# Performance work log

Hardware: AMD Instinct MI355X
Metric: run time of the kernel (lower is better)

Reference implementation:

```python
import jax, jax.numpy as jnp
import numpy as np

H = 8          # n_heads
THRESH = 0.5   # edge pruning threshold
LN_EPS = 1e-5


def setup_inputs() -> dict:
    key = jax.random.key(0)
    ks = jax.random.split(key, 24)
    B, S, D = 8, 128, 256
    N = S + 1
    hd = D // H

    def lin(k, fan_in, fan_out, gain=1.0):
        # xavier_uniform-ish init, stored as [in, out] (y = x @ W + b)
        lim = gain * np.sqrt(6.0 / (fan_in + fan_out))
        return jax.random.uniform(k, (fan_in, fan_out), jnp.float32, -lim, lim)

    g = 1.0 / np.sqrt(2.0)
    return {
        "desc": jax.random.normal(ks[0], (B, S, D), jnp.float32),
        "nv": jax.random.normal(ks[1], (B, N, D), jnp.float32),
        "W_gt": lin(ks[2], D, D), "b_gt": jnp.zeros((D,), jnp.float32),
        "topo_bias": jnp.zeros((1,), jnp.float32),
        "W_q": lin(ks[3], D, D, g), "b_q": jnp.zeros((D,), jnp.float32),
        "W_k": lin(ks[4], D, D, g), "b_k": jnp.zeros((D,), jnp.float32),
        "W_v": lin(ks[5], D, D, g), "b_v": jnp.zeros((D,), jnp.float32),
        "W_e1": lin(ks[6], 2 * D, D), "b_e1": jnp.zeros((D,), jnp.float32),
        "ln_g": jnp.ones((D,), jnp.float32), "ln_b": jnp.zeros((D,), jnp.float32),
        "W_e2": lin(ks[7], D, D), "b_e2": jnp.zeros((D,), jnp.float32),
        "w_attn": lin(ks[8], 3 * hd, 1, g)[:, 0], "b_attn": jnp.zeros((), jnp.float32),
        "W_o": lin(ks[9], D, D, g), "b_o": jnp.zeros((D,), jnp.float32),
    }


def _forward(desc, nv, W_gt, b_gt, topo_bias, W_q, b_q, W_k, b_k, W_v, b_v,
             W_e1, b_e1, ln_g, ln_b, W_e2, b_e2, w_attn, b_attn, W_o, b_o):
    B, N, D = nv.shape
    S = N - 1
    hd = D // H

    # 1. global topology
    d = desc @ W_gt + b_gt                                   # [B,S,D]
    dn = d / jnp.linalg.norm(d, axis=-1, keepdims=True)
    global_top = jax.nn.sigmoid(jnp.einsum('bid,bjd->bij', dn, dn) + topo_bias[0])

    # 2. sample-wise similarity
    var = nv[:, 1:, :]
    vn = var / jnp.linalg.norm(var, axis=-1, keepdims=True)
    sample_sim = jnp.einsum('bid,bjd->bij', vn, vn)
    adj_mat = global_top * sample_sim

    # 3. remove self-connection, squash
    diag_mask = 1.0 - jnp.eye(S, dtype=adj_mat.dtype)
    adj = jax.nn.sigmoid(adj_mat * diag_mask)

    # 4. straight-through edge pruning (frozen=False path)
    hard = (adj > THRESH).astype(adj.dtype)
    adj = hard - jax.lax.stop_gradient(adj) + adj

    # 5. edge attributes: Linear(concat(d_i,d_j)) decomposed into two matmuls
    a = d @ W_e1[:D]                                          # node_i part [B,S,D]
    b_ = d @ W_e1[D:]                                         # node_j part [B,S,D]
    pre = jnp.zeros((B, N, N, D), dtype=d.dtype)
    pre = pre.at[:, 1:, 1:].set(a[:, :, None, :] + b_[:, None, :, :])
    cls = a + b_                                              # concat(d_j,d_j) rows
    pre = pre.at[:, 0, 1:].set(cls).at[:, 1:, 0].set(cls)
    pre = pre + b_e1                                          # (0,0) entry = bias only (zeros input)
    mu = pre.mean(-1, keepdims=True)
    vr = ((pre - mu) ** 2).mean(-1, keepdims=True)
    e = jax.nn.relu((pre - mu) * jax.lax.rsqrt(vr + LN_EPS) * ln_g + ln_b)
    e = e @ W_e2 + b_e2                                       # [B,N,N,D]
    e = e.reshape(B, N, N, H, hd).transpose(0, 3, 1, 2, 4)    # [B,H,N,N,hd]

    # padded adjacency: CLS row attends to all vars, col 0 masked
    na = jnp.zeros((B, N, N), dtype=adj.dtype)
    na = na.at[:, 1:, 1:].set(adj).at[:, 0, 1:].set(1.0)
    e = e * na[:, None, :, :, None]

    # 6. additive attention: attn_proj(concat(q,k,e)) decomposed
    q = (nv @ W_q + b_q).reshape(B, N, H, hd).transpose(0, 2, 1, 3)
    k = (nv @ W_k + b_k).reshape(B, N, H, hd).transpose(0, 2, 1, 3)
    v = (nv @ W_v + b_v).reshape(B, N, H, hd).transpose(0, 2, 1, 3)
    wq, wk, we = w_attn[:hd], w_attn[hd:2 * hd], w_attn[2 * hd:]
    scores = (jnp.einsum('bhid,d->bhi', q, wq)[:, :, :, None]
              + jnp.einsum('bhjd,d->bhj', k, wk)[:, :, None, :]
              + jnp.einsum('bhijd,d->bhij', e, we) + b_attn)
    scores = scores + (na[:, None, :, :] == 0).astype(scores.dtype) * -1e9
    attn = jax.nn.softmax(scores, axis=-1)                    # dropout = identity (eval)

    ctx = jnp.einsum('bhij,bhjd->bhid', attn, v)
    out = ctx.transpose(0, 2, 1, 3).reshape(B, N, D) @ W_o + b_o
    return out, attn


def reference(desc, nv, W_gt, b_gt, topo_bias, W_q, b_q, W_k, b_k, W_v, b_v,
              W_e1, b_e1, ln_g, ln_b, W_e2, b_e2, w_attn, b_attn, W_o, b_o):
    return _forward(desc, nv, W_gt, b_gt, topo_bias, W_q, b_q, W_k, b_k, W_v, b_v,
                    W_e1, b_e1, ln_g, ln_b, W_e2, b_e2, w_attn, b_attn, W_o, b_o)
```

## Files before the change

### kernel.cpp

```cpp
#include <hip/hip_runtime.h>
#include <math.h>

#define BB 8
#define SS 128
#define NN 129
#define DD 256
#define HH 8
#define LN_EPS 1e-5f

#define OFF_A    0
#define OFF_BPT  262144
#define OFF_CPT  524288
#define OFF_VART 786432
#define OFF_V    1048576
#define OFF_SQ   1312768
#define OFF_SK   1321024
#define OFF_MA   1329280
#define OFF_QA   1330304
#define OFF_MB   1331328
#define OFF_QB   1332352
#define OFF_MC   1333376
#define OFF_QC   1334400
#define OFF_U    1335424
#define OFF_UB   1337472
#define OFF_G    1337600
#define OFF_VV   1468672

struct SA {
    float dsc[4][DD];
    float drow[4][DD];
    float4 red[8][4][64];
    float part[24][4];
};
struct SB {
    float rows[2][DD];
    float4 redq[8][2][64];
    float4 redk[8][2][64];
};
union SMA { SA a; SB b; };

__global__ __launch_bounds__(512) void ka_all(
    const float* __restrict__ desc, const float* __restrict__ nv,
    const float* __restrict__ W_gt, const float* __restrict__ b_gt,
    const float* __restrict__ W_e1, const float* __restrict__ b_e1,
    const float* __restrict__ W_q, const float* __restrict__ b_q,
    const float* __restrict__ W_k, const float* __restrict__ b_k,
    const float* __restrict__ W_v, const float* __restrict__ b_v,
    const float* __restrict__ W_e2, const float* __restrict__ b_e2,
    const float* __restrict__ w_attn,
    float* __restrict__ a, float* __restrict__ bp_t, float* __restrict__ cp_t,
    float* __restrict__ var_t, float* __restrict__ v,
    float* __restrict__ sq, float* __restrict__ sk,
    float* __restrict__ ma, float* __restrict__ qa, float* __restrict__ mb,
    float* __restrict__ qb, float* __restrict__ mc, float* __restrict__ qc,
    float* __restrict__ U, float* __restrict__ ubias) {
    __shared__ SMA sm;
    const int bx = blockIdx.x, t = threadIdx.x;

    if (bx < 256) {
        SA& S = sm.a;
        const int b = bx >> 5, s0 = (bx & 31) * 4;
        const int dq = t & 63, kh = t >> 6;
        for (int e = t; e < 4 * DD; e += 512)
            S.dsc[e >> 8][e & 255] = desc[(size_t)(b * SS + s0 + (e >> 8)) * DD + (e & 255)];
        __syncthreads();
        {
            float4 acc[4];
#pragma unroll
            for (int r = 0; r < 4; r++) acc[r] = make_float4(0.f, 0.f, 0.f, 0.f);
            const int kb = kh * 32;
#pragma unroll 4
            for (int k = kb; k < kb + 32; k++) {
                float4 w = *(const float4*)&W_gt[k * DD + 4 * dq];
#pragma unroll
                for (int r = 0; r < 4; r++) {
                    float x = S.dsc[r][k];
                    acc[r].x = fmaf(x, w.x, acc[r].x); acc[r].y = fmaf(x, w.y, acc[r].y);
                    acc[r].z = fmaf(x, w.z, acc[r].z); acc[r].w = fmaf(x, w.w, acc[r].w);
                }
            }
#pragma unroll
            for (int r = 0; r < 4; r++) S.red[kh][r][dq] = acc[r];
        }
        __syncthreads();
        for (int e = t; e < 4 * DD; e += 512) {
            int r = e >> 8, d2 = e & 255;
            float s = b_gt[d2];
#pragma unroll
            for (int kk = 0; kk < 8; kk++) s += ((const float*)S.red[kk][r])[d2];
            S.drow[r][d2] = s;
        }
        __syncthreads();
        {
            float4 acc[4];
#pragma unroll
            for (int r = 0; r < 4; r++) acc[r] = make_float4(0.f, 0.f, 0.f, 0.f);
            const int kb = kh * 32;
#pragma unroll 4
            for (int k = kb; k < kb + 32; k++) {
                float4 w = *(const float4*)&W_e1[k * DD + 4 * dq];
#pragma unroll
                for (int r = 0; r < 4; r++) {
                    float x = S.drow[r][k];
                    acc[r].x = fmaf(x, w.x, acc[r].x); acc[r].y = fmaf(x, w.y, acc[r].y);
                    acc[r].z = fmaf(x, w.z, acc[r].z); acc[r].w = fmaf(x, w.w, acc[r].w);
                }
            }
#pragma unroll
            for (int r = 0; r < 4; r++) S.red[kh][r][dq] = acc[r];
        }
        __syncthreads();
        float avf[4];
        if (t < 256) {
            const int d2 = t;
#pragma unroll
            for (int r = 0; r < 4; r++) {
                float s = 0.f;
#pragma unroll
                for (int kk = 0; kk < 8; kk++) s += ((const float*)S.red[kk][r])[d2];
                avf[r] = s;
                a[(size_t)(b * SS + s0 + r) * DD + d2] = s;
            }
        }
        __syncthreads();
        {
            float4 acc[4];
#pragma unroll
            for (int r = 0; r < 4; r++) acc[r] = make_float4(0.f, 0.f, 0.f, 0.f);
            const int kb = kh * 32;
#pragma unroll 4
            for (int k = kb; k < kb + 32; k++) {
                float4 w = *(const float4*)&W_e1[(DD + k) * DD + 4 * dq];
#pragma unroll
                for (int r = 0; r < 4; r++) {
                    float x = S.drow[r][k];
                    acc[r].x = fmaf(x, w.x, acc[r].x); acc[r].y = fmaf(x, w.y, acc[r].y);
                    acc[r].z = fmaf(x, w.z, acc[r].z); acc[r].w = fmaf(x, w.w, acc[r].w);
                }
            }
#pragma unroll
            for (int r = 0; r < 4; r++) S.red[kh][r][dq] = acc[r];
        }
        __syncthreads();
        if (t < 256) {
            const int d2 = t;
            float bvf[4], cvf[4];
            float be1 = b_e1[d2];
#pragma unroll
            for (int r = 0; r < 4; r++) {
                float s = 0.f;
#pragma unroll
                for (int kk = 0; kk < 8; kk++) s += ((const float*)S.red[kk][r])[d2];
                bvf[r] = s + be1; cvf[r] = avf[r] + bvf[r];
            }
            float4 f4;
            f4.x = bvf[0]; f4.y = bvf[1]; f4.z = bvf[2]; f4.w = bvf[3];
            *(float4*)(bp_t + (size_t)(b * DD + d2) * SS + s0) = f4;
            f4.x = cvf[0]; f4.y = cvf[1]; f4.z = cvf[2]; f4.w = cvf[3];
            *(float4*)(cp_t + (size_t)(b * DD + d2) * SS + s0) = f4;
            float nvv[4];
#pragma unroll
            for (int r = 0; r < 4; r++) nvv[r] = nv[(size_t)(b * NN + 1 + s0 + r) * DD + d2];
            f4.x = nvv[0]; f4.y = nvv[1]; f4.z = nvv[2]; f4.w = nvv[3];
            *(float4*)(var_t + (size_t)(b * DD + d2) * SS + s0) = f4;
            float vals[24];
#pragma unroll
            for (int r = 0; r < 4; r++) {
                vals[r * 6 + 0] = avf[r]; vals[r * 6 + 1] = avf[r] * avf[r];
                vals[r * 6 + 2] = bvf[r]; vals[r * 6 + 3] = bvf[r] * bvf[r];
                vals[r * 6 + 4] = cvf[r]; vals[r * 6 + 5] = cvf[r] * cvf[r];
            }
            int lane = t & 63, wid = t >> 6;
#pragma unroll
            for (int vv = 0; vv < 24; vv++) {
                float x = vals[vv];
                for (int o = 32; o; o >>= 1) x += __shfl_xor(x, o, 64);
                if (lane == 0) S.part[vv][wid] = x;
            }
        }
        __syncthreads();
        if (t < 24) {
            float ssum = (S.part[t][0] + S.part[t][1]) + (S.part[t][2] + S.part[t][3]);
            int st = t % 6;
            int row = b * SS + s0 + t / 6;
            float m = ssum * (1.f / DD);
            float* dstp = (st == 0) ? ma : (st == 1) ? qa : (st == 2) ? mb
                         : (st == 3) ? qb : (st == 4) ? mc : qc;
            dstp[row] = m;
        }
    } else if (bx < 776) {
        SB& S = sm.b;
        const int idx = bx - 256;
        const int b = idx / 65, n0 = (idx % 65) * 2;
        const int dq = t & 63, kh = t >> 6;
        {
            int r = t >> 8, d2 = t & 255;
            int n = n0 + r; if (n >= NN) n = NN - 1;
            S.rows[r][d2] = nv[(size_t)(b * NN + n) * DD + d2];
        }
        __syncthreads();
        {
            float4 aq[2], ak[2];
#pragma unroll
            for (int r = 0; r < 2; r++) { aq[r] = make_float4(0.f, 0.f, 0.f, 0.f); ak[r] = aq[r]; }
            const int kb = kh * 32;
#pragma unroll 4
            for (int k = kb; k < kb + 32; k++) {
                float4 wq = *(const float4*)&W_q[k * DD + 4 * dq];
                float4 wk = *(const float4*)&W_k[k * DD + 4 * dq];
#pragma unroll
                for (int r = 0; r < 2; r++) {
                    float x = S.rows[r][k];
                    aq[r].x = fmaf(x, wq.x, aq[r].x); aq[r].y = fmaf(x, wq.y, aq[r].y);
                    aq[r].z = fmaf(x, wq.z, aq[r].z); aq[r].w = fmaf(x, wq.w, aq[r].w);
                    ak[r].x = fmaf(x, wk.x, ak[r].x); ak[r].y = fmaf(x, wk.y, ak[r].y);
                    ak[r].z = fmaf(x, wk.z, ak[r].z); ak[r].w = fmaf(x, wk.w, ak[r].w);
                }
            }
#pragma unroll
            for (int r = 0; r < 2; r++) { S.redq[kh][r][dq] = aq[r]; S.redk[kh][r][dq] = ak[r]; }
        }
        __syncthreads();
        {
            const int d2 = t & 255, r = t >> 8;
            const int n = n0 + r;
            float qf = b_q[d2], kf = b_k[d2];
#pragma unroll
            for (int kk = 0; kk < 8; kk++) {
                qf += ((const float*)S.redq[kk][r])[d2];
                kf += ((const float*)S.redk[kk][r])[d2];
            }
            float xq = qf * w_attn[d2 & 31];
            float xk = kf * w_attn[32 + (d2 & 31)];
#pragma unroll
            for (int o = 16; o; o >>= 1) { xq += __shfl_xor(xq, o, 32); xk += __shfl_xor(xk, o, 32); }
            if ((d2 & 31) == 0 && n < NN) {
                sq[(size_t)(b * HH + (d2 >> 5)) * NN + n] = xq;
                sk[(size_t)(b * HH + (d2 >> 5)) * NN + n] = xk;
            }
        }
        __syncthreads();
        {
            float4 av[2];
#pragma unroll
            for (int r = 0; r < 2; r++) av[r] = make_float4(0.f, 0.f, 0.f, 0.f);
            const int kb = kh * 32;
#pragma unroll 4
            for (int k = kb; k < kb + 32; k++) {
                float4 wv = *(const float4*)&W_v[k * DD + 4 * dq];
#pragma unroll
                for (int r = 0; r < 2; r++) {
                    float x = S.rows[r][k];
                    av[r].x = fmaf(x, wv.x, av[r].x); av[r].y = fmaf(x, wv.y, av[r].y);
                    av[r].z = fmaf(x, wv.z, av[r].z); av[r].w = fmaf(x, wv.w, av[r].w);
                }
            }
#pragma unroll
            for (int r = 0; r < 2; r++) S.redq[kh][r][dq] = av[r];
        }
        __syncthreads();
        {
            const int d2 = t & 255, r = t >> 8;
            const int n = n0 + r;
            if (n < NN) {
                float vf = b_v[d2];
#pragma unroll
                for (int kk = 0; kk < 8; kk++) vf += ((const float*)S.redq[kk][r])[d2];
                v[(size_t)(b * NN + n) * DD + d2] = vf;
            }
        }
    } else {
        const int ri = bx - 776;
        if (t < 256) {
            const int c = t;
            const float wec = w_attn[64 + (c & 31)];
#pragma unroll
            for (int rr = 0; rr < 4; rr++) {
                int r = ri * 4 + rr;
                float x = W_e2[(size_t)r * DD + c] * wec;
#pragma unroll
                for (int o = 16; o; o >>= 1) x += __shfl_xor(x, o, 32);
                if ((c & 31) == 0) U[r * HH + (c >> 5)] = x;
            }
            if (ri == 0) {
                float x = b_e2[c] * wec;
#pragma unroll
                for (int o = 16; o; o >>= 1) x += __shfl_xor(x, o, 32);
                if ((c & 31) == 0) ubias[c >> 5] = x;
            }
        }
    }
}

__global__ __launch_bounds__(256) void kgram(
    const float* __restrict__ a, const float* __restrict__ bp_t,
    const float* __restrict__ nv, const float* __restrict__ var_t,
    float* __restrict__ G, float* __restrict__ VV) {
    const int bx = blockIdx.x, t = threadIdx.x;
    const bool isG = bx < 128;
    const int idx = isG ? bx : bx - 128;
    const int b = idx >> 4, tl = idx & 15;
    const int i0 = (tl >> 1) * 16, j0 = (tl & 1) * 64;
    const float* Asrc = isG ? (a + ((size_t)b * SS + i0) * DD)
                            : (nv + ((size_t)b * NN + 1 + i0) * DD);
    const float* Bt = (isG ? bp_t : var_t) + (size_t)b * DD * SS;
    float* C = (isG ? G : VV) + (size_t)b * SS * SS;
    __shared__ __attribute__((aligned(16))) float Al[16][DD];
    for (int e = t; e < 16 * DD / 4; e += 256) {
        int r = e >> 6, c4 = e & 63;
        *(float4*)&Al[r][c4 * 4] = *(const float4*)&Asrc[(size_t)r * DD + c4 * 4];
    }
    __syncthreads();
    const int dg = t & 3, jl = t >> 2;
    float acc[16] = {0.f, 0.f, 0.f, 0.f, 0.f, 0.f, 0.f, 0.f,
                     0.f, 0.f, 0.f, 0.f, 0.f, 0.f, 0.f, 0.f};
    const float* bp = Bt + (size_t)(dg * 64) * SS + j0 + jl;
#pragma unroll 4
    for (int dd = 0; dd < 64; dd++) {
        float bvv = bp[(size_t)dd * SS];
        int d = dg * 64 + dd;
#pragma unroll
        for (int i = 0; i < 16; i++) acc[i] = fmaf(Al[i][d], bvv, acc[i]);
    }
#pragma unroll
    for (int i = 0; i < 16; i++) {
        acc[i] += __shfl_xor(acc[i], 1);
        acc[i] += __shfl_xor(acc[i], 2);
    }
    if (dg == 0) {
#pragma unroll
        for (int i = 0; i < 16; i++) C[(size_t)(i0 + i) * SS + j0 + jl] = acc[i];
    }
}

__global__ __launch_bounds__(256) void kb4(
    const float* __restrict__ a, const float* __restrict__ bp_t, const float* __restrict__ cp_t,
    const float* __restrict__ ma, const float* __restrict__ qa,
    const float* __restrict__ mb, const float* __restrict__ qb,
    const float* __restrict__ mc, const float* __restrict__ qc,
    const float* __restrict__ G, const float* __restrict__ VV,
    const float* __restrict__ sq, const float* __restrict__ sk,
    const float* __restrict__ ln_g, const float* __restrict__ ln_b,
    const float* __restrict__ U, const float* __restrict__ ubias,
    const float* __restrict__ b_attn,
    float* __restrict__ attn) {
    const int it = blockIdx.x, b = blockIdx.y;
    const int i0 = it * 2;
    const int t = threadIdx.x;
    const int dg = t >> 6, jl = t & 63;
    __shared__ float Arow[2][DD];
    __shared__ __attribute__((aligned(8))) float2 lnsm[DD];
    __shared__ __attribute__((aligned(16))) float4 Usm[DD][2];
    __shared__ __attribute__((aligned(8))) float rsm[2][SS], nmm[2][SS], mkm[2][SS], pnm[2][SS];
    __shared__ float skm[HH * NN];
    __shared__ float sqb[2][HH], ubm[HH];
    __shared__ float sc[2][HH][NN + 3];
    __shared__ __attribute__((aligned(8))) float red[4][2][HH][SS];

    {
        int ic0 = i0, ic1 = (i0 + 1 < NN) ? i0 + 1 : NN - 1;
        Arow[0][t] = (ic0 >= 1) ? a[((size_t)b * SS + ic0 - 1) * DD + t] : 0.f;
        Arow[1][t] = (ic1 >= 1) ? a[((size_t)b * SS + ic1 - 1) * DD + t] : 0.f;
        float2 g; g.x = ln_g[t]; g.y = ln_b[t]; lnsm[t] = g;
        Usm[t][0] = *(const float4*)&U[t * HH];
        Usm[t][1] = *(const float4*)&U[t * HH + 4];
        for (int e = t; e < HH * NN; e += 256) skm[e] = sk[(size_t)b * HH * NN + e];
        if (t < 16) {
            int il = t >> 3, h = t & 7;
            int i = i0 + il; if (i > NN - 1) i = NN - 1;
            sqb[il][h] = sq[(size_t)b * HH * NN + h * NN + i] + b_attn[0];
        }
        if (t < HH) ubm[t] = ubias[t];
    }
    __syncthreads();
    if (t < SS) {
        const int j = t;
#pragma unroll
        for (int il = 0; il < 2; il++) {
            int i = i0 + il; if (i > NN - 1) i = NN - 1;
            float rs, nm, mk, pen;
            if (i == 0) {
                float mu = mc[b * SS + j], q2 = qc[b * SS + j];
                rs = rsqrtf(q2 - mu * mu + LN_EPS); nm = -mu * rs; mk = 1.f; pen = 0.f;
            } else {
                float cr = G[((size_t)b * SS + i - 1) * SS + j];
                float dv = VV[((size_t)b * SS + i - 1) * SS + j];
                float muA = ma[b * SS + i - 1], qA = qa[b * SS + i - 1];
                float muB = mb[b * SS + j], qB = qb[b * SS + j];
                float mu = muA + muB;
                float var = qA + qB + 2.f * cr * (1.f / DD) - mu * mu;
                rs = rsqrtf(var + LN_EPS); nm = -mu * rs;
                mk = ((i - 1) != j && dv > 0.f) ? 1.f : 0.f;
                pen = (mk == 0.f) ? -1e9f : 0.f;
            }
            rsm[il][j] = rs; nmm[il][j] = nm; mkm[il][j] = mk; pnm[il][j] = pen;
        }
    }
    __syncthreads();
    float acc[2][HH][2];
#pragma unroll
    for (int il = 0; il < 2; il++)
#pragma unroll
        for (int h = 0; h < HH; h++) { acc[il][h][0] = 0.f; acc[il][h][1] = 0.f; }
    {
        const float* Bb = bp_t + ((size_t)b * DD + dg * 64) * SS + 2 * jl;
        float2 r0 = *(const float2*)&rsm[0][2 * jl];
        float2 n0 = *(const float2*)&nmm[0][2 * jl];
        float2 r1 = *(const float2*)&rsm[1][2 * jl];
        float2 n1 = *(const float2*)&nmm[1][2 * jl];
        if (i0 != 0) {
#pragma unroll 4
            for (int dd = 0; dd < 64; dd++) {
                const int d = dg * 64 + dd;
                float2 bv = *(const float2*)(Bb + (size_t)dd * SS);
                float A0 = Arow[0][d], A1 = Arow[1][d];
                float2 gb = lnsm[d];
                float4 u0 = Usm[d][0], u1 = Usm[d][1];
                float y0 = fmaf(A0 + bv.x, r0.x, n0.x); y0 = fmaf(y0, gb.x, gb.y);
                float y1 = fmaf(A0 + bv.y, r0.y, n0.y); y1 = fmaf(y1, gb.x, gb.y);
                float e0 = fmaxf(y0, 0.f), e1 = fmaxf(y1, 0.f);
                float z0 = fmaf(A1 + bv.x, r1.x, n1.x); z0 = fmaf(z0, gb.x, gb.y);
                float z1 = fmaf(A1 + bv.y, r1.y, n1.y); z1 = fmaf(z1, gb.x, gb.y);
                float f0 = fmaxf(z0, 0.f), f1 = fmaxf(z1, 0.f);
                acc[0][0][0] = fmaf(e0, u0.x, acc[0][0][0]); acc[0][0][1] = fmaf(e1, u0.x, acc[0][0][1]);
                acc[0][1][0] = fmaf(e0, u0.y, acc[0][1][0]); acc[0][1][1] = fmaf(e1, u0.y, acc[0][1][1]);
                acc[0][2][0] = fmaf(e0, u0.z, acc[0][2][0]); acc[0][2][1] = fmaf(e1, u0.z, acc[0][2][1]);
                acc[0][3][0] = fmaf(e0, u0.w, acc[0][3][0]); acc[0][3][1] = fmaf(e1, u0.w, acc[0][3][1]);
                acc[0][4][0] = fmaf(e0, u1.x, acc[0][4][0]); acc[0][4][1] = fmaf(e1, u1.x, acc[0][4][1]);
                acc[0][5][0] = fmaf(e0, u1.y, acc[0][5][0]); acc[0][5][1] = fmaf(e1, u1.y, acc[0][5][1]);
                acc[0][6][0] = fmaf(e0, u1.z, acc[0][6][0]); acc[0][6][1] = fmaf(e1, u1.z, acc[0][6][1]);
                acc[0][7][0] = fmaf(e0, u1.w, acc[0][7][0]); acc[0][7][1] = fmaf(e1, u1.w, acc[0][7][1]);
                acc[1][0][0] = fmaf(f0, u0.x, acc[1][0][0]); acc[1][0][1] = fmaf(f1, u0.x, acc[1][0][1]);
                acc[1][1][0] = fmaf(f0, u0.y, acc[1][1][0]); acc[1][1][1] = fmaf(f1, u0.y, acc[1][1][1]);
                acc[1][2][0] = fmaf(f0, u0.z, acc[1][2][0]); acc[1][2][1] = fmaf(f1, u0.z, acc[1][2][1]);
                acc[1][3][0] = fmaf(f0, u0.w, acc[1][3][0]); acc[1][3][1] = fmaf(f1, u0.w, acc[1][3][1]);
                acc[1][4][0] = fmaf(f0, u1.x, acc[1][4][0]); acc[1][4][1] = fmaf(f1, u1.x, acc[1][4][1]);
                acc[1][5][0] = fmaf(f0, u1.y, acc[1][5][0]); acc[1][5][1] = fmaf(f1, u1.y, acc[1][5][1]);
                acc[1][6][0] = fmaf(f0, u1.z, acc[1][6][0]); acc[1][6][1] = fmaf(f1, u1.z, acc[1][6][1]);
                acc[1][7][0] = fmaf(f0, u1.w, acc[1][7][0]); acc[1][7][1] = fmaf(f1, u1.w, acc[1][7][1]);
            }
        } else {
            const float* Bc = cp_t + ((size_t)b * DD + dg * 64) * SS + 2 * jl;
#pragma unroll 4
            for (int dd = 0; dd < 64; dd++) {
                const int d = dg * 64 + dd;
                float2 bA = *(const float2*)(Bc + (size_t)dd * SS);
                float2 bB = *(const float2*)(Bb + (size_t)dd * SS);
                float A0 = Arow[0][d], A1 = Arow[1][d];
                float2 gb = lnsm[d];
                float4 u0 = Usm[d][0], u1 = Usm[d][1];
                float y0 = fmaf(A0 + bA.x, r0.x, n0.x); y0 = fmaf(y0, gb.x, gb.y);
                float y1 = fmaf(A0 + bA.y, r0.y, n0.y); y1 = fmaf(y1, gb.x, gb.y);
                float e0 = fmaxf(y0, 0.f), e1 = fmaxf(y1, 0.f);
                float z0 = fmaf(A1 + bB.x, r1.x, n1.x); z0 = fmaf(z0, gb.x, gb.y);
                float z1 = fmaf(A1 + bB.y, r1.y, n1.y); z1 = fmaf(z1, gb.x, gb.y);
                float f0 = fmaxf(z0, 0.f), f1 = fmaxf(z1, 0.f);
                acc[0][0][0] = fmaf(e0, u0.x, acc[0][0][0]); acc[0][0][1] = fmaf(e1, u0.x, acc[0][0][1]);
                acc[0][1][0] = fmaf(e0, u0.y, acc[0][1][0]); acc[0][1][1] = fmaf(e1, u0.y, acc[0][1][1]);
                acc[0][2][0] = fmaf(e0, u0.z, acc[0][2][0]); acc[0][2][1] = fmaf(e1, u0.z, acc[0][2][1]);
                acc[0][3][0] = fmaf(e0, u0.w, acc[0][3][0]); acc[0][3][1] = fmaf(e1, u0.w, acc[0][3][1]);
                acc[0][4][0] = fmaf(e0, u1.x, acc[0][4][0]); acc[0][4][1] = fmaf(e1, u1.x, acc[0][4][1]);
                acc[0][5][0] = fmaf(e0, u1.y, acc[0][5][0]); acc[0][5][1] = fmaf(e1, u1.y, acc[0][5][1]);
                acc[0][6][0] = fmaf(e0, u1.z, acc[0][6][0]); acc[0][6][1] = fmaf(e1, u1.z, acc[0][6][1]);
                acc[0][7][0] = fmaf(e0, u1.w, acc[0][7][0]); acc[0][7][1] = fmaf(e1, u1.w, acc[0][7][1]);
                acc[1][0][0] = fmaf(f0, u0.x, acc[1][0][0]); acc[1][0][1] = fmaf(f1, u0.x, acc[1][0][1]);
                acc[1][1][0] = fmaf(f0, u0.y, acc[1][1][0]); acc[1][1][1] = fmaf(f1, u0.y, acc[1][1][1]);
                acc[1][2][0] = fmaf(f0, u0.z, acc[1][2][0]); acc[1][2][1] = fmaf(f1, u0.z, acc[1][2][1]);
                acc[1][3][0] = fmaf(f0, u0.w, acc[1][3][0]); acc[1][3][1] = fmaf(f1, u0.w, acc[1][3][1]);
                acc[1][4][0] = fmaf(f0, u1.x, acc[1][4][0]); acc[1][4][1] = fmaf(f1, u1.x, acc[1][4][1]);
                acc[1][5][0] = fmaf(f0, u1.y, acc[1][5][0]); acc[1][5][1] = fmaf(f1, u1.y, acc[1][5][1]);
                acc[1][6][0] = fmaf(f0, u1.z, acc[1][6][0]); acc[1][6][1] = fmaf(f1, u1.z, acc[1][6][1]);
                acc[1][7][0] = fmaf(f0, u1.w, acc[1][7][0]); acc[1][7][1] = fmaf(f1, u1.w, acc[1][7][1]);
            }
        }
    }
#pragma unroll
    for (int il = 0; il < 2; il++)
#pragma unroll
        for (int h = 0; h < HH; h++) {
            float2 w; w.x = acc[il][h][0]; w.y = acc[il][h][1];
            *(float2*)&red[dg][il][h][2 * jl] = w;
        }
    __syncthreads();
    for (int e = t; e < 2 * HH * SS; e += 256) {
        int il = e >> 10, h = (e >> 7) & 7, j = e & 127;
        float s = (red[0][il][h][j] + red[1][il][h][j]) + (red[2][il][h][j] + red[3][il][h][j]);
        sc[il][h][1 + j] = sqb[il][h] + skm[h * NN + 1 + j] + (s + ubm[h]) * mkm[il][j] + pnm[il][j];
    }
    if (t < 16) { int il = t >> 3, h = t & 7; sc[il][h][0] = sqb[il][h] + skm[h * NN] - 1e9f; }
    __syncthreads();
    {
        const int row = t >> 4, l = t & 15;
        const int il = row >> 3, h = row & 7;
        const int i = i0 + il;
        float m = -INFINITY;
        for (int j = l; j < NN; j += 16) m = fmaxf(m, sc[il][h][j]);
#pragma unroll
        for (int o = 8; o; o >>= 1) m = fmaxf(m, __shfl_xor(m, o, 16));
        float s = 0.f;
        for (int j = l; j < NN; j += 16) { float e = __expf(sc[il][h][j] - m); sc[il][h][j] = e; s += e; }
#pragma unroll
        for (int o = 8; o; o >>= 1) s += __shfl_xor(s, o, 16);
        float inv = 1.f / s;
        if (i < NN) {
            float* arow = attn + (((size_t)b * HH + h) * NN + i) * NN;
            for (int j = l; j < NN; j += 16) arow[j] = sc[il][h][j] * inv;
        }
    }
}

__global__ __launch_bounds__(512) void kc4(
    const float* __restrict__ attn, const float* __restrict__ v,
    const float* __restrict__ W_o, const float* __restrict__ b_o,
    float* __restrict__ out) {
    const int b = blockIdx.y, i0 = blockIdx.x * 4;
    const int t = threadIdx.x;
    __shared__ float ar[4][HH * 132];
    __shared__ float red[2][4][DD];
    __shared__ float csm[4][DD];
    for (int e = t; e < 4 * HH * NN; e += 512) {
        int il = e / (HH * NN), rem = e - il * (HH * NN);
        int h = rem / NN, j = rem - h * NN;
        int i = i0 + il; if (i >= NN) i = NN - 1;
        ar[il][h * 132 + j] = attn[(((size_t)b * HH + h) * NN + i) * NN + j];
    }
    __syncthreads();
    {
        const int d = t & 255, jh = t >> 8;
        const int h = d >> 5;
        float c0 = 0.f, c1 = 0.f, c2 = 0.f, c3 = 0.f;
        const float* vp = v + (size_t)b * NN * DD + d;
        const int j0 = jh * 65, j1 = jh ? NN : 65;
#pragma unroll 4
        for (int j = j0; j < j1; j++) {
            float vv = vp[(size_t)j * DD];
            c0 = fmaf(ar[0][h * 132 + j], vv, c0);
            c1 = fmaf(ar[1][h * 132 + j], vv, c1);
            c2 = fmaf(ar[2][h * 132 + j], vv, c2);
            c3 = fmaf(ar[3][h * 132 + j], vv, c3);
        }
        red[jh][0][d] = c0; red[jh][1][d] = c1; red[jh][2][d] = c2; red[jh][3][d] = c3;
    }
    __syncthreads();
    for (int e = t; e < 4 * DD; e += 512) {
        int il = e >> 8, d = e & 255;
        csm[il][d] = red[0][il][d] + red[1][il][d];
    }
    __syncthreads();
    {
        const int c = t & 255, kh = t >> 8;
        float o0 = 0.f, o1 = 0.f, o2 = 0.f, o3 = 0.f;
        const int kb = kh * 128;
#pragma unroll 8
        for (int k = kb; k < kb + 128; k++) {
            float w = W_o[(size_t)k * DD + c];
            o0 = fmaf(csm[0][k], w, o0); o1 = fmaf(csm[1][k], w, o1);
            o2 = fmaf(csm[2][k], w, o2); o3 = fmaf(csm[3][k], w, o3);
        }
        red[kh][0][c] = o0; red[kh][1][c] = o1; red[kh][2][c] = o2; red[kh][3][c] = o3;
    }
    __syncthreads();
    for (int e = t; e < 4 * DD; e += 512) {
        int il = e >> 8, d = e & 255;
        int i = i0 + il;
        if (i < NN)
            out[((size_t)b * NN + i) * DD + d] = red[0][il][d] + red[1][il][d] + b_o[d];
    }
}

extern "C" void kernel_launch(void* const* d_in, const int* in_sizes, int n_in,
                              void* d_out, int out_size, void* d_ws, size_t ws_size,
                              hipStream_t stream) {
    const float* desc   = (const float*)d_in[0];
    const float* nv     = (const float*)d_in[1];
    const float* W_gt   = (const float*)d_in[2];
    const float* b_gt   = (const float*)d_in[3];
    const float* W_q    = (const float*)d_in[5];
    const float* b_q    = (const float*)d_in[6];
    const float* W_k    = (const float*)d_in[7];
    const float* b_k    = (const float*)d_in[8];
    const float* W_v    = (const float*)d_in[9];
    const float* b_v    = (const float*)d_in[10];
    const float* W_e1   = (const float*)d_in[11];
    const float* b_e1   = (const float*)d_in[12];
    const float* ln_g   = (const float*)d_in[13];
    const float* ln_b   = (const float*)d_in[14];
    const float* W_e2   = (const float*)d_in[15];
    const float* b_e2   = (const float*)d_in[16];
    const float* w_attn = (const float*)d_in[17];
    const float* b_attn = (const float*)d_in[18];
    const float* W_o    = (const float*)d_in[19];
    const float* b_o    = (const float*)d_in[20];

    float* ws   = (float*)d_ws;
    float* a    = ws + OFF_A;
    float* bp_t = ws + OFF_BPT;
    float* cp_t = ws + OFF_CPT;
    float* vart = ws + OFF_VART;
    float* v    = ws + OFF_V;
    float* sq   = ws + OFF_SQ;
    float* sk   = ws + OFF_SK;
    float* ma   = ws + OFF_MA;
    float* qa   = ws + OFF_QA;
    float* mb   = ws + OFF_MB;
    float* qb   = ws + OFF_QB;
    float* mc   = ws + OFF_MC;
    float* qc   = ws + OFF_QC;
    float* U    = ws + OFF_U;
    float* ub   = ws + OFF_UB;
    float* G    = ws + OFF_G;
    float* VV   = ws + OFF_VV;

    float* out  = (float*)d_out;
    float* attn = (float*)d_out + (size_t)BB * NN * DD;

    ka_all<<<dim3(840), dim3(512), 0, stream>>>(
        desc, nv, W_gt, b_gt, W_e1, b_e1, W_q, b_q, W_k, b_k, W_v, b_v,
        W_e2, b_e2, w_attn,
        a, bp_t, cp_t, vart, v, sq, sk, ma, qa, mb, qb, mc, qc, U, ub);
    kgram<<<dim3(256), dim3(256), 0, stream>>>(a, bp_t, nv, vart, G, VV);
    kb4<<<dim3(65, BB), dim3(256), 0, stream>>>(
        a, bp_t, cp_t, ma, qa, mb, qb, mc, qc, G, VV, sq, sk,
        ln_g, ln_b, U, ub, b_attn, attn);
    kc4<<<dim3(33, BB), dim3(512), 0, stream>>>(attn, v, W_o, b_o, out);
}
```

Measured before the change: 185.3 us.

## Fuse gram, attention-score and output-projection kernels into one per-row-pair kernel

Drops the separate gram-matrix kernel and the attention-times-V/output-projection kernel, folding both into the score kernel. Each block now computes its own G and VV rows directly from the transposed operands, keeps the softmax probabilities in shared memory, and runs the context and W_o projections locally. This removes two launches and the global round trips for G/VV and for re-reading attn. The cost is more redundant work per block: bp_t and var_t are reread for every row pair, W_o is reloaded by 520 blocks instead of 264, and shared-memory pressure rises.

Result: slower. 191.2 us (+3.2%).

```diff
diff --git a/kernel.cpp b/kernel.cpp
--- a/kernel.cpp
+++ b/kernel.cpp
@@ -23,8 +23,6 @@
 #define OFF_QC   1334400
 #define OFF_U    1335424
 #define OFF_UB   1337472
-#define OFF_G    1337600
-#define OFF_VV   1468672
 
 struct SA {
     float dsc[4][DD];
@@ -292,75 +290,40 @@
     }
 }
 
-__global__ __launch_bounds__(256) void kgram(
-    const float* __restrict__ a, const float* __restrict__ bp_t,
-    const float* __restrict__ nv, const float* __restrict__ var_t,
-    float* __restrict__ G, float* __restrict__ VV) {
-    const int bx = blockIdx.x, t = threadIdx.x;
-    const bool isG = bx < 128;
-    const int idx = isG ? bx : bx - 128;
-    const int b = idx >> 4, tl = idx & 15;
-    const int i0 = (tl >> 1) * 16, j0 = (tl & 1) * 64;
-    const float* Asrc = isG ? (a + ((size_t)b * SS + i0) * DD)
-                            : (nv + ((size_t)b * NN + 1 + i0) * DD);
-    const float* Bt = (isG ? bp_t : var_t) + (size_t)b * DD * SS;
-    float* C = (isG ? G : VV) + (size_t)b * SS * SS;
-    __shared__ __attribute__((aligned(16))) float Al[16][DD];
-    for (int e = t; e < 16 * DD / 4; e += 256) {
-        int r = e >> 6, c4 = e & 63;
-        *(float4*)&Al[r][c4 * 4] = *(const float4*)&Asrc[(size_t)r * DD + c4 * 4];
-    }
-    __syncthreads();
-    const int dg = t & 3, jl = t >> 2;
-    float acc[16] = {0.f, 0.f, 0.f, 0.f, 0.f, 0.f, 0.f, 0.f,
-                     0.f, 0.f, 0.f, 0.f, 0.f, 0.f, 0.f, 0.f};
-    const float* bp = Bt + (size_t)(dg * 64) * SS + j0 + jl;
-#pragma unroll 4
-    for (int dd = 0; dd < 64; dd++) {
-        float bvv = bp[(size_t)dd * SS];
-        int d = dg * 64 + dd;
-#pragma unroll
-        for (int i = 0; i < 16; i++) acc[i] = fmaf(Al[i][d], bvv, acc[i]);
-    }
-#pragma unroll
-    for (int i = 0; i < 16; i++) {
-        acc[i] += __shfl_xor(acc[i], 1);
-        acc[i] += __shfl_xor(acc[i], 2);
-    }
-    if (dg == 0) {
-#pragma unroll
-        for (int i = 0; i < 16; i++) C[(size_t)(i0 + i) * SS + j0 + jl] = acc[i];
-    }
-}
-
-__global__ __launch_bounds__(256) void kb4(
+__global__ __launch_bounds__(256) void kmega(
     const float* __restrict__ a, const float* __restrict__ bp_t, const float* __restrict__ cp_t,
+    const float* __restrict__ var_t, const float* __restrict__ nv,
+    const float* __restrict__ v,
     const float* __restrict__ ma, const float* __restrict__ qa,
     const float* __restrict__ mb, const float* __restrict__ qb,
     const float* __restrict__ mc, const float* __restrict__ qc,
-    const float* __restrict__ G, const float* __restrict__ VV,
     const float* __restrict__ sq, const float* __restrict__ sk,
     const float* __restrict__ ln_g, const float* __restrict__ ln_b,
     const float* __restrict__ U, const float* __restrict__ ubias,
     const float* __restrict__ b_attn,
-    float* __restrict__ attn) {
+    const float* __restrict__ W_o, const float* __restrict__ b_o,
+    float* __restrict__ attn, float* __restrict__ out) {
     const int it = blockIdx.x, b = blockIdx.y;
     const int i0 = it * 2;
     const int t = threadIdx.x;
     const int dg = t >> 6, jl = t & 63;
     __shared__ float Arow[2][DD];
+    __shared__ float Vrow[2][DD];
     __shared__ __attribute__((aligned(8))) float2 lnsm[DD];
     __shared__ __attribute__((aligned(16))) float4 Usm[DD][2];
     __shared__ __attribute__((aligned(8))) float rsm[2][SS], nmm[2][SS], mkm[2][SS], pnm[2][SS];
     __shared__ float skm[HH * NN];
     __shared__ float sqb[2][HH], ubm[HH];
     __shared__ float sc[2][HH][NN + 3];
-    __shared__ __attribute__((aligned(8))) float red[4][2][HH][SS];
+    __shared__ __attribute__((aligned(16))) float red[4][2][HH][SS];
+    __shared__ float csm[2][DD];
 
     {
         int ic0 = i0, ic1 = (i0 + 1 < NN) ? i0 + 1 : NN - 1;
         Arow[0][t] = (ic0 >= 1) ? a[((size_t)b * SS + ic0 - 1) * DD + t] : 0.f;
         Arow[1][t] = (ic1 >= 1) ? a[((size_t)b * SS + ic1 - 1) * DD + t] : 0.f;
+        Vrow[0][t] = nv[((size_t)b * NN + ic0) * DD + t];
+        Vrow[1][t] = nv[((size_t)b * NN + ic1) * DD + t];
         float2 g; g.x = ln_g[t]; g.y = ln_b[t]; lnsm[t] = g;
         Usm[t][0] = *(const float4*)&U[t * HH];
         Usm[t][1] = *(const float4*)&U[t * HH + 4];
@@ -373,6 +336,32 @@
         if (t < HH) ubm[t] = ubias[t];
     }
     __syncthreads();
+
+    {
+        float cr[2][2] = {{0.f, 0.f}, {0.f, 0.f}}, dvv[2][2] = {{0.f, 0.f}, {0.f, 0.f}};
+        const float* bc = bp_t + ((size_t)b * DD + dg * 64) * SS + 2 * jl;
+        const float* vc = var_t + ((size_t)b * DD + dg * 64) * SS + 2 * jl;
+#pragma unroll 4
+        for (int dd = 0; dd < 64; dd++) {
+            float2 bv = *(const float2*)(bc + (size_t)dd * SS);
+            float2 vv = *(const float2*)(vc + (size_t)dd * SS);
+            const int d = dg * 64 + dd;
+            float A0 = Arow[0][d], A1 = Arow[1][d];
+            float V0 = Vrow[0][d], V1 = Vrow[1][d];
+            cr[0][0] = fmaf(A0, bv.x, cr[0][0]); cr[0][1] = fmaf(A0, bv.y, cr[0][1]);
+            cr[1][0] = fmaf(A1, bv.x, cr[1][0]); cr[1][1] = fmaf(A1, bv.y, cr[1][1]);
+            dvv[0][0] = fmaf(V0, vv.x, dvv[0][0]); dvv[0][1] = fmaf(V0, vv.y, dvv[0][1]);
+            dvv[1][0] = fmaf(V1, vv.x, dvv[1][0]); dvv[1][1] = fmaf(V1, vv.y, dvv[1][1]);
+        }
+#pragma unroll
+        for (int il = 0; il < 2; il++) {
+            float2 w0; w0.x = cr[il][0]; w0.y = cr[il][1];
+            float2 w1; w1.x = dvv[il][0]; w1.y = dvv[il][1];
+            *(float2*)&red[dg][il][0][2 * jl] = w0;
+            *(float2*)&red[dg][il][1][2 * jl] = w1;
+        }
+    }
+    __syncthreads();
     if (t < SS) {
         const int j = t;
 #pragma unroll
@@ -383,8 +372,8 @@
                 float mu = mc[b * SS + j], q2 = qc[b * SS + j];
                 rs = rsqrtf(q2 - mu * mu + LN_EPS); nm = -mu * rs; mk = 1.f; pen = 0.f;
             } else {
-                float cr = G[((size_t)b * SS + i - 1) * SS + j];
-                float dv = VV[((size_t)b * SS + i - 1) * SS + j];
+                float cr = (red[0][il][0][j] + red[1][il][0][j]) + (red[2][il][0][j] + red[3][il][0][j]);
+                float dv = (red[0][il][1][j] + red[1][il][1][j]) + (red[2][il][1][j] + red[3][il][1][j]);
                 float muA = ma[b * SS + i - 1], qA = qa[b * SS + i - 1];
                 float muB = mb[b * SS + j], qB = qb[b * SS + j];
                 float mu = muA + muB;
@@ -498,73 +487,86 @@
 #pragma unroll
         for (int o = 8; o; o >>= 1) m = fmaxf(m, __shfl_xor(m, o, 16));
         float s = 0.f;
-        for (int j = l; j < NN; j += 16) { float e = __expf(sc[il][h][j] - m); sc[il][h][j] = e; s += e; }
+        float ev[9];
+        int cnt = 0;
+        for (int j = l; j < NN; j += 16) { float e = __expf(sc[il][h][j] - m); ev[cnt++] = e; s += e; }
 #pragma unroll
         for (int o = 8; o; o >>= 1) s += __shfl_xor(s, o, 16);
         float inv = 1.f / s;
-        if (i < NN) {
-            float* arow = attn + (((size_t)b * HH + h) * NN + i) * NN;
-            for (int j = l; j < NN; j += 16) arow[j] = sc[il][h][j] * inv;
-        }
-    }
-}
-
-__global__ __launch_bounds__(512) void kc4(
-    const float* __restrict__ attn, const float* __restrict__ v,
-    const float* __restrict__ W_o, const float* __restrict__ b_o,
-    float* __restrict__ out) {
-    const int b = blockIdx.y, i0 = blockIdx.x * 4;
-    const int t = threadIdx.x;
-    __shared__ float ar[4][HH * 132];
-    __shared__ float red[2][4][DD];
-    __shared__ float csm[4][DD];
-    for (int e = t; e < 4 * HH * NN; e += 512) {
-        int il = e / (HH * NN), rem = e - il * (HH * NN);
-        int h = rem / NN, j = rem - h * NN;
-        int i = i0 + il; if (i >= NN) i = NN - 1;
-        ar[il][h * 132 + j] = attn[(((size_t)b * HH + h) * NN + i) * NN + j];
-    }
-    __syncthreads();
-    {
-        const int d = t & 255, jh = t >> 8;
-        const int h = d >> 5;
-        float c0 = 0.f, c1 = 0.f, c2 = 0.f, c3 = 0.f;
-        const float* vp = v + (size_t)b * NN * DD + d;
-        const int j0 = jh * 65, j1 = jh ? NN : 65;
-#pragma unroll 4
-        for (int j = j0; j < j1; j++) {
-            float vv = vp[(size_t)j * DD];
-            c0 = fmaf(ar[0][h * 132 + j], vv, c0);
-            c1 = fmaf(ar[1][h * 132 + j], vv, c1);
-            c2 = fmaf(ar[2][h * 132 + j], vv, c2);
-            c3 = fmaf(ar[3][h * 132 + j], vv, c3);
-        }
-        red[jh][0][d] = c0; red[jh][1][d] = c1; red[jh][2][d] = c2; red[jh][3][d] = c3;
-    }
-    __syncthreads();
-    for (int e = t; e < 4 * DD; e += 512) {
-        int il = e >> 8, d = e & 255;
-        csm[il][d] = red[0][il][d] + red[1][il][d];
-    }
-    __syncthreads();
-    {
-        const int c = t & 255, kh = t >> 8;
-        float o0 = 0.f, o1 = 0.f, o2 = 0.f, o3 = 0.f;
-        const int kb = kh * 128;
-#pragma unroll 8
-        for (int k = kb; k < kb + 128; k++) {
-            float w = W_o[(size_t)k * DD + c];
-            o0 = fmaf(csm[0][k], w, o0); o1 = fmaf(csm[1][k], w, o1);
-            o2 = fmaf(csm[2][k], w, o2); o3 = fmaf(csm[3][k], w, o3);
-        }
-        red[kh][0][c] = o0; red[kh][1][c] = o1; red[kh][2][c] = o2; red[kh][3][c] = o3;
-    }
-    __syncthreads();
-    for (int e = t; e < 4 * DD; e += 512) {
-        int il = e >> 8, d = e & 255;
-        int i = i0 + il;
-        if (i < NN)
-            out[((size_t)b * NN + i) * DD + d] = red[0][il][d] + red[1][il][d] + b_o[d];
+        float* arow = attn + (((size_t)b * HH + h) * NN + i) * NN;
+        cnt = 0;
+        for (int j = l; j < NN; j += 16) {
+            float p = ev[cnt++] * inv;
+            sc[il][h][j] = p;
+            if (i < NN) arow[j] = p;
+        }
+    }
+    __syncthreads();
+    {
+        const int dq = t & 63, jg = t >> 6;
+        const int h = dq >> 3;
+        float ca[2][4] = {{0.f, 0.f, 0.f, 0.f}, {0.f, 0.f, 0.f, 0.f}};
+#pragma unroll 4
+        for (int jj = 0; jj < 33; jj++) {
+            int j = jg * 33 + jj;
+            if (j < NN) {
+                float4 vv = *(const float4*)&v[((size_t)b * NN + j) * DD + 4 * dq];
+                float p0 = sc[0][h][j], p1 = sc[1][h][j];
+                ca[0][0] = fmaf(p0, vv.x, ca[0][0]); ca[0][1] = fmaf(p0, vv.y, ca[0][1]);
+                ca[0][2] = fmaf(p0, vv.z, ca[0][2]); ca[0][3] = fmaf(p0, vv.w, ca[0][3]);
+                ca[1][0] = fmaf(p1, vv.x, ca[1][0]); ca[1][1] = fmaf(p1, vv.y, ca[1][1]);
+                ca[1][2] = fmaf(p1, vv.z, ca[1][2]); ca[1][3] = fmaf(p1, vv.w, ca[1][3]);
+            }
+        }
+        float* redf = &red[0][0][0][0];
+#pragma unroll
+        for (int il = 0; il < 2; il++) {
+            float4 w; w.x = ca[il][0]; w.y = ca[il][1]; w.z = ca[il][2]; w.w = ca[il][3];
+            *(float4*)&redf[jg * 512 + il * 256 + 4 * dq] = w;
+        }
+    }
+    __syncthreads();
+    {
+        const float* redf = &red[0][0][0][0];
+#pragma unroll
+        for (int il = 0; il < 2; il++)
+            csm[il][t] = (redf[il * 256 + t] + redf[512 + il * 256 + t])
+                       + (redf[1024 + il * 256 + t] + redf[1536 + il * 256 + t]);
+    }
+    __syncthreads();
+    {
+        const int cq = t & 63, kg = t >> 6;
+        float o[2][4] = {{0.f, 0.f, 0.f, 0.f}, {0.f, 0.f, 0.f, 0.f}};
+#pragma unroll 4
+        for (int kk = 0; kk < 64; kk++) {
+            int k = kg * 64 + kk;
+            float4 w = *(const float4*)&W_o[(size_t)k * DD + 4 * cq];
+            float c0 = csm[0][k], c1 = csm[1][k];
+            o[0][0] = fmaf(c0, w.x, o[0][0]); o[0][1] = fmaf(c0, w.y, o[0][1]);
+            o[0][2] = fmaf(c0, w.z, o[0][2]); o[0][3] = fmaf(c0, w.w, o[0][3]);
+            o[1][0] = fmaf(c1, w.x, o[1][0]); o[1][1] = fmaf(c1, w.y, o[1][1]);
+            o[1][2] = fmaf(c1, w.z, o[1][2]); o[1][3] = fmaf(c1, w.w, o[1][3]);
+        }
+        float* redf = &red[0][0][0][0];
+#pragma unroll
+        for (int il = 0; il < 2; il++) {
+            float4 w; w.x = o[il][0]; w.y = o[il][1]; w.z = o[il][2]; w.w = o[il][3];
+            *(float4*)&redf[kg * 512 + il * 256 + 4 * cq] = w;
+        }
+    }
+    __syncthreads();
+    {
+        const float* redf = &red[0][0][0][0];
+        float bo = b_o[t];
+#pragma unroll
+        for (int il = 0; il < 2; il++) {
+            int i = i0 + il;
+            if (i < NN) {
+                float s = (redf[il * 256 + t] + redf[512 + il * 256 + t])
+                        + (redf[1024 + il * 256 + t] + redf[1536 + il * 256 + t]) + bo;
+                out[((size_t)b * NN + i) * DD + t] = s;
+            }
+        }
     }
 }
 
@@ -608,8 +610,6 @@
     float* qc   = ws + OFF_QC;
     float* U    = ws + OFF_U;
     float* ub   = ws + OFF_UB;
-    float* G    = ws + OFF_G;
-    float* VV   = ws + OFF_VV;
 
     float* out  = (float*)d_out;
     float* attn = (float*)d_out + (size_t)BB * NN * DD;
@@ -618,9 +618,7 @@
         desc, nv, W_gt, b_gt, W_e1, b_e1, W_q, b_q, W_k, b_k, W_v, b_v,
         W_e2, b_e2, w_attn,
         a, bp_t, cp_t, vart, v, sq, sk, ma, qa, mb, qb, mc, qc, U, ub);
-    kgram<<<dim3(256), dim3(256), 0, stream>>>(a, bp_t, nv, vart, G, VV);
-    kb4<<<dim3(65, BB), dim3(256), 0, stream>>>(
-        a, bp_t, cp_t, ma, qa, mb, qb, mc, qc, G, VV, sq, sk,
-        ln_g, ln_b, U, ub, b_attn, attn);
-    kc4<<<dim3(33, BB), dim3(512), 0, stream>>>(attn, v, W_o, b_o, out);
+    kmega<<<dim3(65, BB), dim3(256), 0, stream>>>(
+        a, bp_t, cp_t, vart, nv, v, ma, qa, mb, qb, mc, qc, sq, sk,
+        ln_g, ln_b, U, ub, b_attn, W_o, b_o, attn, out);
 }
```
